# Optimization experiments

Hardware: AMD Instinct MI355X
Metric: run time of the kernel (lower is better)

## Reference

```python
import jax, jax.numpy as jnp
import numpy as np

BITS = 8
TOPK_PERCENT = 0.1
THRESHOLD = 0.5


def _quantize_per_channel(v, n_bits):
    # scales: abs-max over last dim, clamped, divided by q_max
    q_max = 2 ** (n_bits - 1) - 1
    scales = jnp.max(jnp.abs(v), axis=-1, keepdims=True)
    scales = jnp.clip(scales, 1e-5, None) / q_max
    return jnp.clip(jnp.round(v / scales), -q_max - 1, q_max) * scales


def setup_inputs() -> dict:
    key = jax.random.key(0)
    ks = jax.random.split(key, 5)
    B, S, D, H = 4, 2048, 1024, 4096
    return {
        "x": jax.random.normal(ks[0], (B, S, D), dtype=jnp.float32),
        "W1": jax.random.normal(ks[1], (H, D), dtype=jnp.float32) * 0.02,
        "b1": jax.random.normal(ks[2], (H,), dtype=jnp.float32) * 0.02,
        "W2": jax.random.normal(ks[3], (D, H), dtype=jnp.float32) * 0.02,
        "b2": jax.random.normal(ks[4], (D,), dtype=jnp.float32) * 0.02,
    }


def reference(x, W1, b1, W2, b2):
    D = W1.shape[-1]
    H = W1.shape[0]
    topk_rows = int(D * TOPK_PERCENT) + 1  # first-k-columns approximation

    # approximate preactivation using only the first topk_rows input channels
    prod_topk = jnp.einsum('bsk,hk->bsh', x[:, :, :topk_rows], W1[:, :topk_rows]) + b1
    # exact fp preactivation
    prod = jnp.einsum('bsd,hd->bsh', x, W1) + b1

    # quantized path: per-channel quant of x, W1, b1 then matmul
    q_x = _quantize_per_channel(x, BITS)
    q_w = _quantize_per_channel(W1, BITS)
    q_b = _quantize_per_channel(b1, BITS)
    q_pre = jnp.einsum('bsd,hd->bsh', q_x, q_w) + q_b

    # channel selection: channels predicted positive often enough stay fp
    threshold = prod_topk.shape[-1] * THRESHOLD
    num_pos_pred = jnp.sum(prod_topk > 0, axis=(0, 1))  # [H]
    fp_channels = num_pos_pred > threshold              # [H] bool

    h = jnp.where(fp_channels, prod, q_pre)
    h = jax.nn.gelu(h, approximate=False)
    out = jnp.einsum('bsh,dh->bsd', h, W2) + b2
    return out
```

## Files before the change

### kernel.cpp

```cpp
#include <hip/hip_runtime.h>
#include <math.h>
#include <stdint.h>


typedef __bf16 v8bf __attribute__((ext_vector_type(8)));
typedef float v4f __attribute__((ext_vector_type(4)));
typedef unsigned short v8us __attribute__((ext_vector_type(8)));

#define AS_G __attribute__((address_space(1)))
#define AS_L __attribute__((address_space(3)))
#define GLOAD(gp, lp) __builtin_amdgcn_global_load_lds((const AS_G void*)(gp), (AS_L void*)(lp), 16, 0, 0)
#define WAITV(n) asm volatile("s_waitcnt vmcnt(" #n ")" ::: "memory")
#define FENCE() __builtin_amdgcn_sched_barrier(0)
#define BAR() __builtin_amdgcn_s_barrier()

__device__ __forceinline__ unsigned short f2bf(float f) {
    union { float f; unsigned int i; } v; v.f = f;
    unsigned int r = v.i + 0x7fffu + ((v.i >> 16) & 1u);
    return (unsigned short)(r >> 16);
}
__device__ __forceinline__ float gelu_fast(float v) {
    float u = v * (0.79788456080286536f + 0.035677408136300125f * v * v);
    u = fminf(fmaxf(u, -15.f), 15.f);
    float e = __expf(2.0f * u);
    return v * e * __builtin_amdgcn_rcpf(e + 1.0f);
}
__device__ __forceinline__ float gelu_exact(float v) {
    return 0.5f * v * (1.0f + erff(v * 0.70710678118654752440f));
}

template<int NB>
__device__ __forceinline__ void gemm_core8(const unsigned short* __restrict__ A,
                                           const unsigned short* __restrict__ B,
                                           const int K, const int NC,
                                           const int bm0, const int bn0,
                                           unsigned short* lds,
                                           v4f (&acc)[8][NB / 4])
{
    constexpr int NF = NB / 4;
    constexpr int CH = (16 + NB) * 512;
    const int tid  = threadIdx.x;
    const int wave = tid >> 6;
    const int lane = tid & 63;
    const int wm = wave >> 2, wn = wave & 3;
    const int rowInChunk = lane >> 2;
    const int col8 = ((lane & 3) ^ ((lane >> 3) & 3)) * 8;
    const int ldsLane = lane * 8;
    const int R = lane & 15, Q = lane >> 4;
    const int roff = R * 32 + ((Q ^ ((R >> 1) & 3)) * 8);

    const size_t aR0 = (size_t)(bm0 + (2 * wave)     * 16 + rowInChunk) * K + col8;
    const size_t aR1 = (size_t)(bm0 + (2 * wave + 1) * 16 + rowInChunk) * K + col8;
    size_t bR0 = 0, bR1 = 0;
    if constexpr (NB == 16) {
        bR0 = (size_t)(bn0 + (2 * wave)     * 16 + rowInChunk) * K + col8;
        bR1 = (size_t)(bn0 + (2 * wave + 1) * 16 + rowInChunk) * K + col8;
    } else {
        bR0 = (size_t)(bn0 + wave * 16 + rowInChunk) * K + col8;
    }

    auto STAGE = [&](int kc, unsigned short* s) {
        const int k0 = kc * 32;
        GLOAD(A + aR0 + k0, s + (2 * wave) * 512 + ldsLane);
        GLOAD(A + aR1 + k0, s + (2 * wave + 1) * 512 + ldsLane);
        if constexpr (NB == 16) {
            GLOAD(B + bR0 + k0, s + (16 + 2 * wave) * 512 + ldsLane);
            GLOAD(B + bR1 + k0, s + (16 + 2 * wave + 1) * 512 + ldsLane);
        } else {
            GLOAD(B + bR0 + k0, s + (16 + wave) * 512 + ldsLane);
        }
    };
    auto COMPUTE = [&](const unsigned short* s) {
        v8bf af[8], bf[NF];
#pragma unroll
        for (int mf = 0; mf < 8; ++mf)
            af[mf] = *(const v8bf*)&s[(wm * 8 + mf) * 512 + roff];
#pragma unroll
        for (int nf = 0; nf < NF; ++nf)
            bf[nf] = *(const v8bf*)&s[(16 + wn * NF + nf) * 512 + roff];
        __builtin_amdgcn_s_setprio(1);
#pragma unroll
        for (int mf = 0; mf < 8; ++mf)
#pragma unroll
            for (int nf = 0; nf < NF; ++nf)
                acc[mf][nf] = __builtin_amdgcn_mfma_f32_16x16x32_bf16(af[mf], bf[nf], acc[mf][nf], 0, 0, 0);
        __builtin_amdgcn_s_setprio(0);
    };

    unsigned short* const sl3 = lds + 3 * (size_t)CH;
    STAGE(0, lds);
    STAGE(1, lds + CH);
    STAGE(2, lds + 2 * (size_t)CH);
    unsigned short* pc = lds;
    unsigned short* ps = sl3;

    for (int c = 0; c < NC - 3; ++c) {
        STAGE(c + 3, ps);
        if constexpr (NB == 16) WAITV(12); else WAITV(9);
        FENCE(); BAR(); FENCE();
        COMPUTE(pc);
        FENCE(); BAR(); FENCE();
        ps = pc;
        pc = (pc == sl3) ? lds : pc + CH;
    }
    if constexpr (NB == 16) WAITV(8); else WAITV(6);
    FENCE(); BAR(); FENCE();
    COMPUTE(pc);
    FENCE(); BAR(); FENCE();
    pc = (pc == sl3) ? lds : pc + CH;
    if constexpr (NB == 16) WAITV(4); else WAITV(3);
    FENCE(); BAR(); FENCE();
    COMPUTE(pc);
    FENCE(); BAR(); FENCE();
    pc = (pc == sl3) ? lds : pc + CH;
    WAITV(0);
    FENCE(); BAR(); FENCE();
    COMPUTE(pc);
    FENCE(); BAR(); FENCE();
}

__global__ void prep_kernel(const float* __restrict__ x, const float* __restrict__ W1,
                            const float* __restrict__ W2, const float* __restrict__ b1,
                            unsigned short* __restrict__ xb, unsigned short* __restrict__ w1b,
                            unsigned short* __restrict__ w2b,
                            unsigned short* __restrict__ xpad, unsigned short* __restrict__ w1pad,
                            float* __restrict__ s_x, float* __restrict__ s_w,
                            float* __restrict__ s_b, int* __restrict__ counts)
{
    const int b = blockIdx.x, t = threadIdx.x;
    __shared__ float red[4];

    if (b < 16384) {
        const float* src; unsigned short* dst; unsigned short* pad = nullptr; float* sc = nullptr;
        if (b < 8192)       { src = x  + (size_t)b * 1024;            dst = xb  + (size_t)b * 1024;
                              pad = xpad  + (size_t)b * 128;          sc = s_x + b; }
        else if (b < 12288) { int r = b - 8192;  src = W1 + (size_t)r * 1024; dst = w1b + (size_t)r * 1024;
                              pad = w1pad + (size_t)r * 128;          sc = s_w + r; }
        else                { int r = b - 12288; src = W2 + (size_t)r * 1024; dst = w2b + (size_t)r * 1024; }

        float4 v = ((const float4*)src)[t];
        ushort4 u;
        u.x = f2bf(v.x); u.y = f2bf(v.y); u.z = f2bf(v.z); u.w = f2bf(v.w);
        ((ushort4*)dst)[t] = u;
        if (pad && t < 32) {
            int c = t * 4;
            ushort4 p;
            p.x = (c + 0 < 103) ? u.x : (unsigned short)0;
            p.y = (c + 1 < 103) ? u.y : (unsigned short)0;
            p.z = (c + 2 < 103) ? u.z : (unsigned short)0;
            p.w = (c + 3 < 103) ? u.w : (unsigned short)0;
            ((ushort4*)pad)[t] = p;
        }
        if (sc) {
            float m = fmaxf(fmaxf(fabsf(v.x), fabsf(v.y)), fmaxf(fabsf(v.z), fabsf(v.w)));
#pragma unroll
            for (int off = 32; off; off >>= 1) m = fmaxf(m, __shfl_xor(m, off, 64));
            if ((t & 63) == 0) red[t >> 6] = m;
            __syncthreads();
            if (t == 0) {
                m = fmaxf(fmaxf(red[0], red[1]), fmaxf(red[2], red[3]));
                *sc = fmaxf(m, 1e-5f) * (1.0f / 127.0f);
            }
        }
    } else {
        float m = 0.f;
        for (int k = t; k < 4096; k += 256) { m = fmaxf(m, fabsf(b1[k])); counts[k] = 0; }
#pragma unroll
        for (int off = 32; off; off >>= 1) m = fmaxf(m, __shfl_xor(m, off, 64));
        if ((t & 63) == 0) red[t >> 6] = m;
        __syncthreads();
        if (t == 0) {
            m = fmaxf(fmaxf(red[0], red[1]), fmaxf(red[2], red[3]));
            *s_b = fmaxf(m, 1e-5f) * (1.0f / 127.0f);
        }
    }
}

__global__ __launch_bounds__(512, 2)
void gemm1_topk(const unsigned short* __restrict__ xb,
                const unsigned short* __restrict__ w1b,
                const unsigned short* __restrict__ xpad,
                const unsigned short* __restrict__ w1pad,
                const float* __restrict__ b1,
                unsigned short* __restrict__ hbuf,
                int* __restrict__ counts)
{
    __shared__ unsigned short lds[65536];
    v4f acc[8][4];
    v4f z = {0.f, 0.f, 0.f, 0.f};
#pragma unroll
    for (int i = 0; i < 8; ++i)
#pragma unroll
        for (int j = 0; j < 4; ++j) acc[i][j] = z;

    const int bn0 = blockIdx.x * 256, bm0 = blockIdx.y * 256;
    const int tid = threadIdx.x;
    const int lane = tid & 63, wave = tid >> 6;
    const int wm = wave >> 2, wn = wave & 3, q = lane >> 4;

    if (blockIdx.z == 0) {
        gemm_core8<16>(xb, w1b, 1024, 32, bm0, bn0, lds, acc);

        float bvj[4];
#pragma unroll
        for (int nf = 0; nf < 4; ++nf) bvj[nf] = b1[bn0 + wn * 64 + nf * 16 + (lane & 15)];

        unsigned short* slab = lds;
#pragma unroll
        for (int p = 0; p < 4; ++p) {
            __syncthreads();
            if (wm == (p >> 1)) {
                const int mfb = (p & 1) * 4;
#pragma unroll
                for (int mfp = 0; mfp < 4; ++mfp)
#pragma unroll
                    for (int nf = 0; nf < 4; ++nf) {
                        const int colq = wn * 64 + nf * 16 + (lane & 15);
#pragma unroll
                        for (int r = 0; r < 4; ++r)
                            slab[(mfp * 16 + q * 4 + r) * 256 + colq] =
                                f2bf(gelu_fast(acc[mfb + mfp][nf][r] + bvj[nf]));
                    }
            }
            __syncthreads();
#pragma unroll
            for (int s = 0; s < 4; ++s) {
                const int idx = s * 512 + tid;
                const int row = idx >> 5, ch = idx & 31;
                *(v8us*)&hbuf[(size_t)(bm0 + p * 64 + row) * 4096 + bn0 + ch * 8] =
                    *(const v8us*)&slab[row * 256 + ch * 8];
            }
        }
    } else {
        gemm_core8<16>(xpad, w1pad, 128, 4, bm0, bn0, lds, acc);

#pragma unroll
        for (int nf = 0; nf < 4; ++nf) {
            const int n = bn0 + wn * 64 + nf * 16 + (lane & 15);
            const float bv = b1[n];
            int cnt = 0;
#pragma unroll
            for (int mf = 0; mf < 8; ++mf)
#pragma unroll
                for (int r = 0; r < 4; ++r)
                    cnt += (acc[mf][nf][r] + bv > 0.0f) ? 1 : 0;
            cnt += __shfl_xor(cnt, 16, 64);
            cnt += __shfl_xor(cnt, 32, 64);
            if (lane < 16 && cnt) atomicAdd(&counts[n], cnt);
        }
    }
}

__global__ void fixup_kernel(const float* __restrict__ x,
                             const float* __restrict__ W1,
                             const float* __restrict__ b1,
                             const int* __restrict__ counts,
                             const float* __restrict__ s_x,
                             const float* __restrict__ s_w,
                             const float* __restrict__ s_b,
                             unsigned short* __restrict__ hbuf)
{
    const int n = blockIdx.x;
    if (counts[n] > 2048) return;
    __shared__ float qw[1024];
    const float swn = s_w[n];
    for (int k = threadIdx.x; k < 1024; k += 256) {
        float q = nearbyintf(W1[(size_t)n * 1024 + k] / swn);
        qw[k] = fminf(fmaxf(q, -128.f), 127.f) * swn;
    }
    __syncthreads();
    const float sb = *s_b;
    const float bq = fminf(fmaxf(nearbyintf(b1[n] / sb), -128.f), 127.f) * sb;
    for (int m = threadIdx.x; m < 8192; m += 256) {
        const float sxm = s_x[m];
        float a = 0.f;
        for (int k = 0; k < 1024; ++k) {
            float q = nearbyintf(x[(size_t)m * 1024 + k] / sxm);
            a += fminf(fmaxf(q, -128.f), 127.f) * sxm * qw[k];
        }
        hbuf[(size_t)m * 4096 + n] = f2bf(gelu_exact(a + bq));
    }
}

__global__ __launch_bounds__(512, 2)
void gemm2_bias(const unsigned short* __restrict__ hbuf,
                const unsigned short* __restrict__ w2b,
                const float* __restrict__ b2,
                float* __restrict__ out)
{
    __shared__ unsigned short lds[49152];
    v4f acc[8][2];
    v4f z = {0.f, 0.f, 0.f, 0.f};
#pragma unroll
    for (int i = 0; i < 8; ++i)
#pragma unroll
        for (int j = 0; j < 2; ++j) acc[i][j] = z;

    const int bn0 = blockIdx.x * 128, bm0 = blockIdx.y * 256;
    const int tid = threadIdx.x;
    const int lane = tid & 63, wave = tid >> 6;
    const int wm = wave >> 2, wn = wave & 3, q = lane >> 4;

    gemm_core8<8>(hbuf, w2b, 4096, 128, bm0, bn0, lds, acc);

    float bvj[2];
#pragma unroll
    for (int nf = 0; nf < 2; ++nf) bvj[nf] = b2[bn0 + wn * 32 + nf * 16 + (lane & 15)];

    float* slabf = (float*)lds;
#pragma unroll
    for (int p = 0; p < 4; ++p) {
        __syncthreads();
        if (wm == (p >> 1)) {
            const int mfb = (p & 1) * 4;
#pragma unroll
            for (int mfp = 0; mfp < 4; ++mfp)
#pragma unroll
                for (int nf = 0; nf < 2; ++nf) {
                    const int colq = wn * 32 + nf * 16 + (lane & 15);
#pragma unroll
                    for (int r = 0; r < 4; ++r)
                        slabf[(mfp * 16 + q * 4 + r) * 128 + colq] =
                            acc[mfb + mfp][nf][r] + bvj[nf];
                }
        }
        __syncthreads();
#pragma unroll
        for (int s = 0; s < 4; ++s) {
            const int idx = s * 512 + tid;
            const int row = idx >> 5, ch = idx & 31;
            *(float4*)&out[(size_t)(bm0 + p * 64 + row) * 1024 + bn0 + ch * 4] =
                *(const float4*)&slabf[row * 128 + ch * 4];
        }
    }
}

extern "C" void kernel_launch(void* const* d_in, const int* in_sizes, int n_in,
                              void* d_out, int out_size, void* d_ws, size_t ws_size,
                              hipStream_t stream)
{
    const float* x  = (const float*)d_in[0];
    const float* W1 = (const float*)d_in[1];
    const float* b1 = (const float*)d_in[2];
    const float* W2 = (const float*)d_in[3];
    const float* b2 = (const float*)d_in[4];
    float* out = (float*)d_out;

    unsigned short* xb  = (unsigned short*)d_out;
    unsigned short* w1b = (unsigned short*)d_out + (size_t)8192 * 1024;

    char* ws = (char*)d_ws;
    int*   counts = (int*)(ws + 0);
    float* s_x    = (float*)(ws + (64 << 10));
    float* s_w    = (float*)(ws + (96 << 10));
    float* s_b    = (float*)(ws + (112 << 10));
    unsigned short* xpad  = (unsigned short*)(ws + (1 << 20));
    unsigned short* w1pad = (unsigned short*)(ws + (3 << 20));
    unsigned short* w2b   = (unsigned short*)(ws + (4 << 20));
    unsigned short* hbuf  = (unsigned short*)(ws + (12 << 20));

    prep_kernel<<<16385, 256, 0, stream>>>(x, W1, W2, b1, xb, w1b, w2b,
                                           xpad, w1pad, s_x, s_w, s_b, counts);
    gemm1_topk<<<dim3(16, 32, 2), 512, 0, stream>>>(xb, w1b, xpad, w1pad, b1, hbuf, counts);
    fixup_kernel<<<4096, 256, 0, stream>>>(x, W1, b1, counts, s_x, s_w, s_b, hbuf);
    gemm2_bias<<<dim3(8, 32), 512, 0, stream>>>(hbuf, w2b, b2, out);
}
```

Baseline: 300.0 us.

## Restructure GEMM mainloop into double-buffered 64-wide K tiles with interleaved half-steps

Replaces the 4-stage ring of 32-wide K chunks with two 64-wide K tile buffers. Each tile is split into sub-steps where LDS fragment reads, async global-to-LDS loads for future tiles, and MFMA groups over half the N fragments are interleaved between barriers. The aim is finer overlap of memory traffic with matrix math and less LDS-read stalling. In exchange it adds many more barriers per K step and fragile hand-tuned vmcnt waits whose correctness depends on the exact load order.

```diff
diff --git a/kernel.cpp b/kernel.cpp
--- a/kernel.cpp
+++ b/kernel.cpp
@@ -30,93 +30,118 @@
 }
 
 template<int NB>
-__device__ __forceinline__ void gemm_core8(const unsigned short* __restrict__ A,
-                                           const unsigned short* __restrict__ B,
-                                           const int K, const int NC,
-                                           const int bm0, const int bn0,
-                                           unsigned short* lds,
-                                           v4f (&acc)[8][NB / 4])
+__device__ __forceinline__ void gemm_core8p(const unsigned short* __restrict__ A,
+                                            const unsigned short* __restrict__ Bm,
+                                            const int K,
+                                            const int bm0, const int bn0,
+                                            unsigned short* lds,
+                                            v4f (&acc)[8][NB / 4])
 {
     constexpr int NF = NB / 4;
-    constexpr int CH = (16 + NB) * 512;
-    const int tid  = threadIdx.x;
-    const int wave = tid >> 6;
-    const int lane = tid & 63;
+    constexpr int FW = NF / 2;
+    constexpr int TILE = (32 + 2 * NB) * 512;
+    const int tid = threadIdx.x;
+    const int wave = tid >> 6, lane = tid & 63;
     const int wm = wave >> 2, wn = wave & 3;
     const int rowInChunk = lane >> 2;
     const int col8 = ((lane & 3) ^ ((lane >> 3) & 3)) * 8;
     const int ldsLane = lane * 8;
     const int R = lane & 15, Q = lane >> 4;
     const int roff = R * 32 + ((Q ^ ((R >> 1) & 3)) * 8);
-
-    const size_t aR0 = (size_t)(bm0 + (2 * wave)     * 16 + rowInChunk) * K + col8;
-    const size_t aR1 = (size_t)(bm0 + (2 * wave + 1) * 16 + rowInChunk) * K + col8;
-    size_t bR0 = 0, bR1 = 0;
+    const int NT2 = K >> 7;
+
+    unsigned short* const buf0 = lds;
+    unsigned short* const buf1 = lds + TILE;
+
+    const size_t aB0 = (size_t)(bm0 + (2 * wave) * 16 + rowInChunk) * K + col8;
+    const size_t aB1 = aB0 + (size_t)16 * K;
+    size_t bB0, bB1 = 0;
     if constexpr (NB == 16) {
-        bR0 = (size_t)(bn0 + (2 * wave)     * 16 + rowInChunk) * K + col8;
-        bR1 = (size_t)(bn0 + (2 * wave + 1) * 16 + rowInChunk) * K + col8;
+        bB0 = (size_t)(bn0 + (2 * wave) * 16 + rowInChunk) * K + col8;
+        bB1 = bB0 + (size_t)16 * K;
     } else {
-        bR0 = (size_t)(bn0 + wave * 16 + rowInChunk) * K + col8;
-    }
-
-    auto STAGE = [&](int kc, unsigned short* s) {
-        const int k0 = kc * 32;
-        GLOAD(A + aR0 + k0, s + (2 * wave) * 512 + ldsLane);
-        GLOAD(A + aR1 + k0, s + (2 * wave + 1) * 512 + ldsLane);
-        if constexpr (NB == 16) {
-            GLOAD(B + bR0 + k0, s + (16 + 2 * wave) * 512 + ldsLane);
-            GLOAD(B + bR1 + k0, s + (16 + 2 * wave + 1) * 512 + ldsLane);
-        } else {
-            GLOAD(B + bR0 + k0, s + (16 + wave) * 512 + ldsLane);
-        }
-    };
-    auto COMPUTE = [&](const unsigned short* s) {
-        v8bf af[8], bf[NF];
-#pragma unroll
-        for (int mf = 0; mf < 8; ++mf)
-            af[mf] = *(const v8bf*)&s[(wm * 8 + mf) * 512 + roff];
-#pragma unroll
-        for (int nf = 0; nf < NF; ++nf)
-            bf[nf] = *(const v8bf*)&s[(16 + wn * NF + nf) * 512 + roff];
-        __builtin_amdgcn_s_setprio(1);
-#pragma unroll
-        for (int mf = 0; mf < 8; ++mf)
-#pragma unroll
-            for (int nf = 0; nf < NF; ++nf)
-                acc[mf][nf] = __builtin_amdgcn_mfma_f32_16x16x32_bf16(af[mf], bf[nf], acc[mf][nf], 0, 0, 0);
-        __builtin_amdgcn_s_setprio(0);
-    };
-
-    unsigned short* const sl3 = lds + 3 * (size_t)CH;
-    STAGE(0, lds);
-    STAGE(1, lds + CH);
-    STAGE(2, lds + 2 * (size_t)CH);
-    unsigned short* pc = lds;
-    unsigned short* ps = sl3;
-
-    for (int c = 0; c < NC - 3; ++c) {
-        STAGE(c + 3, ps);
-        if constexpr (NB == 16) WAITV(12); else WAITV(9);
-        FENCE(); BAR(); FENCE();
-        COMPUTE(pc);
-        FENCE(); BAR(); FENCE();
-        ps = pc;
-        pc = (pc == sl3) ? lds : pc + CH;
-    }
-    if constexpr (NB == 16) WAITV(8); else WAITV(6);
+        bB0 = (size_t)(bn0 + wave * 16 + rowInChunk) * K + col8;
+    }
+
+    v8bf Ar[8];
+    v8bf Br[FW];
+
+#define STG_A(tl, ks, bufp) { \
+    GLOAD(A + aB0 + (tl) * 64 + (ks) * 32, (bufp) + ((2 * wave) * 2 + (ks)) * 512 + ldsLane); \
+    GLOAD(A + aB1 + (tl) * 64 + (ks) * 32, (bufp) + ((2 * wave + 1) * 2 + (ks)) * 512 + ldsLane); }
+#define STG_B(tl, ks, bufp) { \
+    if constexpr (NB == 16) { \
+        GLOAD(Bm + bB0 + (tl) * 64 + (ks) * 32, (bufp) + 16384 + ((2 * wave) * 2 + (ks)) * 512 + ldsLane); \
+        GLOAD(Bm + bB1 + (tl) * 64 + (ks) * 32, (bufp) + 16384 + ((2 * wave + 1) * 2 + (ks)) * 512 + ldsLane); \
+    } else { \
+        GLOAD(Bm + bB0 + (tl) * 64 + (ks) * 32, (bufp) + 16384 + ((wave) * 2 + (ks)) * 512 + ldsLane); } }
+#define RD_A(bufp, ks) { _Pragma("unroll") \
+    for (int mf = 0; mf < 8; ++mf) \
+        Ar[mf] = *(const v8bf*)&(bufp)[((wm * 8 + mf) * 2 + (ks)) * 512 + roff]; }
+#define RD_B(bufp, ks, fg) { _Pragma("unroll") \
+    for (int nfi = 0; nfi < FW; ++nfi) \
+        Br[nfi] = *(const v8bf*)&(bufp)[16384 + ((wn * NF + (fg) * FW + nfi) * 2 + (ks)) * 512 + roff]; }
+#define MM(fg) \
+    __builtin_amdgcn_s_setprio(1); \
+    _Pragma("unroll") for (int mf = 0; mf < 8; ++mf) { \
+    _Pragma("unroll") for (int nfi = 0; nfi < FW; ++nfi) \
+        acc[mf][(fg) * FW + nfi] = __builtin_amdgcn_mfma_f32_16x16x32_bf16(Ar[mf], Br[nfi], acc[mf][(fg) * FW + nfi], 0, 0, 0); } \
+    __builtin_amdgcn_s_setprio(0);
+#define MIDB FENCE(); BAR(); FENCE();
+#define ENDB FENCE(); BAR(); FENCE();
+#define WVS  { if constexpr (NB == 16) { WAITV(10); } else { WAITV(8); } }
+
+    STG_A(0, 0, buf0); STG_B(0, 0, buf0); STG_A(0, 1, buf0); STG_B(0, 1, buf0);
+    STG_A(1, 0, buf1); STG_B(1, 0, buf1); STG_A(1, 1, buf1);
+    WVS;
     FENCE(); BAR(); FENCE();
-    COMPUTE(pc);
-    FENCE(); BAR(); FENCE();
-    pc = (pc == sl3) ? lds : pc + CH;
-    if constexpr (NB == 16) WAITV(4); else WAITV(3);
-    FENCE(); BAR(); FENCE();
-    COMPUTE(pc);
-    FENCE(); BAR(); FENCE();
-    pc = (pc == sl3) ? lds : pc + CH;
-    WAITV(0);
-    FENCE(); BAR(); FENCE();
-    COMPUTE(pc);
-    FENCE(); BAR(); FENCE();
+
+    for (int i = 0; i < NT2 - 1; ++i) {
+        const int t1 = 2 * i + 1, t2 = 2 * i + 2, t3 = 2 * i + 3;
+        RD_A(buf0, 0); RD_B(buf0, 0, 0); STG_B(t1, 1, buf1);
+        MIDB; MM(0); ENDB;
+        RD_B(buf0, 0, 1); STG_A(t2, 0, buf0);
+        MIDB; MM(1); WVS; ENDB;
+        RD_A(buf0, 1); RD_B(buf0, 1, 0); STG_B(t2, 0, buf0);
+        MIDB; MM(0); ENDB;
+        RD_B(buf0, 1, 1); STG_A(t2, 1, buf0);
+        MIDB; MM(1); WVS; ENDB;
+        RD_A(buf1, 0); RD_B(buf1, 0, 0); STG_B(t2, 1, buf0);
+        MIDB; MM(0); ENDB;
+        RD_B(buf1, 0, 1); STG_A(t3, 0, buf1);
+        MIDB; MM(1); WVS; ENDB;
+        RD_A(buf1, 1); RD_B(buf1, 1, 0); STG_B(t3, 0, buf1);
+        MIDB; MM(0); ENDB;
+        RD_B(buf1, 1, 1); STG_A(t3, 1, buf1);
+        MIDB; MM(1); WVS; ENDB;
+    }
+    {
+        const int tl = NT2 * 2 - 1;
+        RD_A(buf0, 0); RD_B(buf0, 0, 0); STG_B(tl, 1, buf1);
+        MIDB; MM(0); ENDB;
+        RD_B(buf0, 0, 1);
+        MIDB; MM(1); if constexpr (NB == 16) { WAITV(8); } else { WAITV(6); } ENDB;
+        RD_A(buf0, 1); RD_B(buf0, 1, 0);
+        MIDB; MM(0); ENDB;
+        RD_B(buf0, 1, 1);
+        MIDB; MM(1); if constexpr (NB == 16) { WAITV(4); } else { WAITV(3); } ENDB;
+        RD_A(buf1, 0); RD_B(buf1, 0, 0);
+        MIDB; MM(0); ENDB;
+        RD_B(buf1, 0, 1);
+        MIDB; MM(1); WAITV(0); ENDB;
+        RD_A(buf1, 1); RD_B(buf1, 1, 0);
+        MIDB; MM(0); ENDB;
+        RD_B(buf1, 1, 1);
+        MIDB; MM(1); ENDB;
+    }
+#undef STG_A
+#undef STG_B
+#undef RD_A
+#undef RD_B
+#undef MM
+#undef MIDB
+#undef ENDB
+#undef WVS
 }
 
 __global__ void prep_kernel(const float* __restrict__ x, const float* __restrict__ W1,
@@ -199,7 +224,7 @@
     const int wm = wave >> 2, wn = wave & 3, q = lane >> 4;
 
     if (blockIdx.z == 0) {
-        gemm_core8<16>(xb, w1b, 1024, 32, bm0, bn0, lds, acc);
+        gemm_core8p<16>(xb, w1b, 1024, bm0, bn0, lds, acc);
 
         float bvj[4];
 #pragma unroll
@@ -232,7 +257,7 @@
             }
         }
     } else {
-        gemm_core8<16>(xpad, w1pad, 128, 4, bm0, bn0, lds, acc);
+        gemm_core8p<16>(xpad, w1pad, 128, bm0, bn0, lds, acc);
 
 #pragma unroll
         for (int nf = 0; nf < 4; ++nf) {
@@ -301,7 +326,7 @@
     const int lane = tid & 63, wave = tid >> 6;
     const int wm = wave >> 2, wn = wave & 3, q = lane >> 4;
 
-    gemm_core8<8>(hbuf, w2b, 4096, 128, bm0, bn0, lds, acc);
+    gemm_core8p<8>(hbuf, w2b, 4096, bm0, bn0, lds, acc);
 
     float bvj[2];
 #pragma unroll
```

After: 300.3 us. About the same (+0.1%).

## Rework GEMM cores to 4-wave blocks with larger per-wave tiles and triple buffering

Applied to the files above, without the earlier changes.

Replaces the shared 8-wave GEMM core with two specialized 4-wave cores (256 threads). Each wave now computes a larger register tile (8x8 or 8x4 MFMA fragments), and B fragments are read in two halves interleaved with MFMA phases. The pipeline moves from a 4-deep to a 3-deep LDS ring, and gemm2 uses a K-step of 64 per stage. The goal is more operand reuse per LDS read and fewer waves sharing the barrier. In exchange, register pressure rises, each block has fewer waves to hide latency, and there are more barriers per K step.

```diff
diff --git a/kernel.cpp b/kernel.cpp
--- a/kernel.cpp
+++ b/kernel.cpp
@@ -29,94 +29,191 @@
     return 0.5f * v * (1.0f + erff(v * 0.70710678118654752440f));
 }
 
-template<int NB>
-__device__ __forceinline__ void gemm_core8(const unsigned short* __restrict__ A,
-                                           const unsigned short* __restrict__ B,
-                                           const int K, const int NC,
-                                           const int bm0, const int bn0,
-                                           unsigned short* lds,
-                                           v4f (&acc)[8][NB / 4])
-{
-    constexpr int NF = NB / 4;
-    constexpr int CH = (16 + NB) * 512;
-    const int tid  = threadIdx.x;
-    const int wave = tid >> 6;
-    const int lane = tid & 63;
-    const int wm = wave >> 2, wn = wave & 3;
+__device__ __forceinline__ void core_g1(const unsigned short* __restrict__ A,
+                                        const unsigned short* __restrict__ B,
+                                        const int K, const int bm0, const int bn0,
+                                        unsigned short* lds, v4f (&acc)[8][8])
+{
+    const int tid = threadIdx.x;
+    const int wave = tid >> 6, lane = tid & 63;
+    const int wm = wave & 1, wn = wave >> 1;
     const int rowInChunk = lane >> 2;
     const int col8 = ((lane & 3) ^ ((lane >> 3) & 3)) * 8;
     const int ldsLane = lane * 8;
     const int R = lane & 15, Q = lane >> 4;
     const int roff = R * 32 + ((Q ^ ((R >> 1) & 3)) * 8);
-
-    const size_t aR0 = (size_t)(bm0 + (2 * wave)     * 16 + rowInChunk) * K + col8;
-    const size_t aR1 = (size_t)(bm0 + (2 * wave + 1) * 16 + rowInChunk) * K + col8;
-    size_t bR0 = 0, bR1 = 0;
-    if constexpr (NB == 16) {
-        bR0 = (size_t)(bn0 + (2 * wave)     * 16 + rowInChunk) * K + col8;
-        bR1 = (size_t)(bn0 + (2 * wave + 1) * 16 + rowInChunk) * K + col8;
-    } else {
-        bR0 = (size_t)(bn0 + wave * 16 + rowInChunk) * K + col8;
-    }
-
-    auto STAGE = [&](int kc, unsigned short* s) {
-        const int k0 = kc * 32;
-        GLOAD(A + aR0 + k0, s + (2 * wave) * 512 + ldsLane);
-        GLOAD(A + aR1 + k0, s + (2 * wave + 1) * 512 + ldsLane);
-        if constexpr (NB == 16) {
-            GLOAD(B + bR0 + k0, s + (16 + 2 * wave) * 512 + ldsLane);
-            GLOAD(B + bR1 + k0, s + (16 + 2 * wave + 1) * 512 + ldsLane);
-        } else {
-            GLOAD(B + bR0 + k0, s + (16 + wave) * 512 + ldsLane);
-        }
-    };
-    auto COMPUTE = [&](const unsigned short* s) {
-        v8bf af[8], bf[NF];
-#pragma unroll
-        for (int mf = 0; mf < 8; ++mf)
-            af[mf] = *(const v8bf*)&s[(wm * 8 + mf) * 512 + roff];
-#pragma unroll
-        for (int nf = 0; nf < NF; ++nf)
-            bf[nf] = *(const v8bf*)&s[(16 + wn * NF + nf) * 512 + roff];
-        __builtin_amdgcn_s_setprio(1);
-#pragma unroll
-        for (int mf = 0; mf < 8; ++mf)
-#pragma unroll
-            for (int nf = 0; nf < NF; ++nf)
-                acc[mf][nf] = __builtin_amdgcn_mfma_f32_16x16x32_bf16(af[mf], bf[nf], acc[mf][nf], 0, 0, 0);
-        __builtin_amdgcn_s_setprio(0);
-    };
-
-    unsigned short* const sl3 = lds + 3 * (size_t)CH;
-    STAGE(0, lds);
-    STAGE(1, lds + CH);
-    STAGE(2, lds + 2 * (size_t)CH);
+    const int NS = K >> 5;
+
+    size_t aR[4], bR[4];
+#pragma unroll
+    for (int r = 0; r < 4; ++r) {
+        aR[r] = (size_t)(bm0 + (wave * 4 + r) * 16 + rowInChunk) * K + col8;
+        bR[r] = (size_t)(bn0 + (wave * 4 + r) * 16 + rowInChunk) * K + col8;
+    }
+
+    v8bf Ar[8], Br[4];
+
+#define G1_STG(c, s) { _Pragma("unroll") \
+    for (int r = 0; r < 4; ++r) { \
+        GLOAD(A + aR[r] + (c) * 32, (s) + (wave * 4 + r) * 512 + ldsLane); \
+        GLOAD(B + bR[r] + (c) * 32, (s) + 8192 + (wave * 4 + r) * 512 + ldsLane); } }
+#define G1_RDA(s) { _Pragma("unroll") \
+    for (int mf = 0; mf < 8; ++mf) \
+        Ar[mf] = *(const v8bf*)&(s)[(wm * 8 + mf) * 512 + roff]; }
+#define G1_RDB(s, fg) { _Pragma("unroll") \
+    for (int nf = 0; nf < 4; ++nf) \
+        Br[nf] = *(const v8bf*)&(s)[8192 + (wn * 8 + (fg) * 4 + nf) * 512 + roff]; }
+#define G1_MM(fg) \
+    __builtin_amdgcn_s_setprio(1); \
+    _Pragma("unroll") for (int mf = 0; mf < 8; ++mf) { \
+    _Pragma("unroll") for (int nf = 0; nf < 4; ++nf) \
+        acc[mf][(fg) * 4 + nf] = __builtin_amdgcn_mfma_f32_16x16x32_bf16(Ar[mf], Br[nf], acc[mf][(fg) * 4 + nf], 0, 0, 0); } \
+    __builtin_amdgcn_s_setprio(0);
+
     unsigned short* pc = lds;
-    unsigned short* ps = sl3;
-
-    for (int c = 0; c < NC - 3; ++c) {
-        STAGE(c + 3, ps);
-        if constexpr (NB == 16) WAITV(12); else WAITV(9);
-        FENCE(); BAR(); FENCE();
-        COMPUTE(pc);
-        FENCE(); BAR(); FENCE();
-        ps = pc;
-        pc = (pc == sl3) ? lds : pc + CH;
-    }
-    if constexpr (NB == 16) WAITV(8); else WAITV(6);
-    FENCE(); BAR(); FENCE();
-    COMPUTE(pc);
-    FENCE(); BAR(); FENCE();
-    pc = (pc == sl3) ? lds : pc + CH;
-    if constexpr (NB == 16) WAITV(4); else WAITV(3);
-    FENCE(); BAR(); FENCE();
-    COMPUTE(pc);
-    FENCE(); BAR(); FENCE();
-    pc = (pc == sl3) ? lds : pc + CH;
-    WAITV(0);
-    FENCE(); BAR(); FENCE();
-    COMPUTE(pc);
-    FENCE(); BAR(); FENCE();
+    unsigned short* pn = lds + 16384;
+    unsigned short* ps = lds + 32768;
+
+    G1_STG(0, pc); G1_STG(1, pn);
+    WAITV(8);
+    FENCE(); BAR(); FENCE();
+
+    for (int c = 0; c < NS - 2; ++c) {
+        G1_RDA(pc); G1_RDB(pc, 0); G1_STG(c + 2, ps);
+        FENCE(); BAR(); FENCE();
+        G1_MM(0);
+        FENCE(); BAR(); FENCE();
+        G1_RDB(pc, 1);
+        FENCE(); BAR(); FENCE();
+        G1_MM(1); WAITV(8);
+        FENCE(); BAR(); FENCE();
+        unsigned short* t = pc; pc = pn; pn = ps; ps = t;
+    }
+    G1_RDA(pc); G1_RDB(pc, 0);
+    FENCE(); BAR(); FENCE();
+    G1_MM(0);
+    FENCE(); BAR(); FENCE();
+    G1_RDB(pc, 1);
+    FENCE(); BAR(); FENCE();
+    G1_MM(1); WAITV(0);
+    FENCE(); BAR(); FENCE();
+    { unsigned short* t = pc; pc = pn; pn = ps; ps = t; }
+    G1_RDA(pc); G1_RDB(pc, 0);
+    FENCE(); BAR(); FENCE();
+    G1_MM(0);
+    FENCE(); BAR(); FENCE();
+    G1_RDB(pc, 1);
+    FENCE(); BAR(); FENCE();
+    G1_MM(1);
+    FENCE(); BAR(); FENCE();
+#undef G1_STG
+#undef G1_RDA
+#undef G1_RDB
+#undef G1_MM
+}
+
+__device__ __forceinline__ void core_g2(const unsigned short* __restrict__ A,
+                                        const unsigned short* __restrict__ B,
+                                        const int K, const int bm0, const int bn0,
+                                        unsigned short* lds, v4f (&acc)[8][4])
+{
+    const int tid = threadIdx.x;
+    const int wave = tid >> 6, lane = tid & 63;
+    const int wm = wave & 1, wn = wave >> 1;
+    const int rowInChunk = lane >> 2;
+    const int col8 = ((lane & 3) ^ ((lane >> 3) & 3)) * 8;
+    const int ldsLane = lane * 8;
+    const int R = lane & 15, Q = lane >> 4;
+    const int roff = R * 32 + ((Q ^ ((R >> 1) & 3)) * 8);
+    const int NS = K >> 6;
+
+    size_t aR[4], bR[2];
+#pragma unroll
+    for (int r = 0; r < 4; ++r)
+        aR[r] = (size_t)(bm0 + (wave * 4 + r) * 16 + rowInChunk) * K + col8;
+#pragma unroll
+    for (int r = 0; r < 2; ++r)
+        bR[r] = (size_t)(bn0 + (wave * 2 + r) * 16 + rowInChunk) * K + col8;
+
+    v8bf Ar[8], Br[2];
+
+#define G2_STG(c, s) { _Pragma("unroll") \
+    for (int r = 0; r < 4; ++r) { _Pragma("unroll") \
+        for (int ks = 0; ks < 2; ++ks) \
+            GLOAD(A + aR[r] + (c) * 64 + ks * 32, (s) + ((wave * 4 + r) * 2 + ks) * 512 + ldsLane); } \
+    _Pragma("unroll") \
+    for (int r = 0; r < 2; ++r) { _Pragma("unroll") \
+        for (int ks = 0; ks < 2; ++ks) \
+            GLOAD(B + bR[r] + (c) * 64 + ks * 32, (s) + 16384 + ((wave * 2 + r) * 2 + ks) * 512 + ldsLane); } }
+#define G2_RDA(s, ks) { _Pragma("unroll") \
+    for (int mf = 0; mf < 8; ++mf) \
+        Ar[mf] = *(const v8bf*)&(s)[((wm * 8 + mf) * 2 + (ks)) * 512 + roff]; }
+#define G2_RDB(s, ks, fg) { _Pragma("unroll") \
+    for (int nf = 0; nf < 2; ++nf) \
+        Br[nf] = *(const v8bf*)&(s)[16384 + ((wn * 4 + (fg) * 2 + nf) * 2 + (ks)) * 512 + roff]; }
+#define G2_MM(fg) \
+    __builtin_amdgcn_s_setprio(1); \
+    _Pragma("unroll") for (int mf = 0; mf < 8; ++mf) { \
+    _Pragma("unroll") for (int nf = 0; nf < 2; ++nf) \
+        acc[mf][(fg) * 2 + nf] = __builtin_amdgcn_mfma_f32_16x16x32_bf16(Ar[mf], Br[nf], acc[mf][(fg) * 2 + nf], 0, 0, 0); } \
+    __builtin_amdgcn_s_setprio(0);
+#define G2_PH(s, ks, fg) \
+    FENCE(); BAR(); FENCE(); \
+    G2_MM(fg); \
+    FENCE(); BAR(); FENCE();
+
+    unsigned short* pc = lds;
+    unsigned short* pn = lds + 24576;
+    unsigned short* ps = lds + 49152;
+
+    G2_STG(0, pc); G2_STG(1, pn);
+    WAITV(12);
+    FENCE(); BAR(); FENCE();
+
+    for (int c = 0; c < NS - 2; ++c) {
+        G2_RDA(pc, 0); G2_RDB(pc, 0, 0); G2_STG(c + 2, ps);
+        FENCE(); BAR(); FENCE();
+        G2_MM(0);
+        FENCE(); BAR(); FENCE();
+        G2_RDB(pc, 0, 1);
+        FENCE(); BAR(); FENCE();
+        G2_MM(1);
+        FENCE(); BAR(); FENCE();
+        G2_RDA(pc, 1); G2_RDB(pc, 1, 0);
+        FENCE(); BAR(); FENCE();
+        G2_MM(0);
+        FENCE(); BAR(); FENCE();
+        G2_RDB(pc, 1, 1);
+        FENCE(); BAR(); FENCE();
+        G2_MM(1); WAITV(12);
+        FENCE(); BAR(); FENCE();
+        unsigned short* t = pc; pc = pn; pn = ps; ps = t;
+    }
+    for (int c = 0; c < 2; ++c) {
+        G2_RDA(pc, 0); G2_RDB(pc, 0, 0);
+        FENCE(); BAR(); FENCE();
+        G2_MM(0);
+        FENCE(); BAR(); FENCE();
+        G2_RDB(pc, 0, 1);
+        FENCE(); BAR(); FENCE();
+        G2_MM(1);
+        FENCE(); BAR(); FENCE();
+        G2_RDA(pc, 1); G2_RDB(pc, 1, 0);
+        FENCE(); BAR(); FENCE();
+        G2_MM(0);
+        FENCE(); BAR(); FENCE();
+        G2_RDB(pc, 1, 1);
+        FENCE(); BAR(); FENCE();
+        G2_MM(1);
+        if (c == 0) { WAITV(0); }
+        FENCE(); BAR(); FENCE();
+        unsigned short* t = pc; pc = pn; pn = ps; ps = t;
+    }
+#undef G2_STG
+#undef G2_RDA
+#undef G2_RDB
+#undef G2_MM
+#undef G2_PH
 }
 
 __global__ void prep_kernel(const float* __restrict__ x, const float* __restrict__ W1,
@@ -176,7 +273,7 @@
     }
 }
 
-__global__ __launch_bounds__(512, 2)
+__global__ __launch_bounds__(256, 1)
 void gemm1_topk(const unsigned short* __restrict__ xb,
                 const unsigned short* __restrict__ w1b,
                 const unsigned short* __restrict__ xpad,
@@ -185,25 +282,26 @@
                 unsigned short* __restrict__ hbuf,
                 int* __restrict__ counts)
 {
-    __shared__ unsigned short lds[65536];
-    v4f acc[8][4];
+    __shared__ unsigned short lds[49152];
+    v4f acc[8][8];
     v4f z = {0.f, 0.f, 0.f, 0.f};
 #pragma unroll
     for (int i = 0; i < 8; ++i)
 #pragma unroll
-        for (int j = 0; j < 4; ++j) acc[i][j] = z;
+        for (int j = 0; j < 8; ++j) acc[i][j] = z;
 
     const int bn0 = blockIdx.x * 256, bm0 = blockIdx.y * 256;
     const int tid = threadIdx.x;
     const int lane = tid & 63, wave = tid >> 6;
-    const int wm = wave >> 2, wn = wave & 3, q = lane >> 4;
+    const int wm = wave & 1, wn = wave >> 1, q = lane >> 4;
+    const int R = lane & 15;
 
     if (blockIdx.z == 0) {
-        gemm_core8<16>(xb, w1b, 1024, 32, bm0, bn0, lds, acc);
-
-        float bvj[4];
-#pragma unroll
-        for (int nf = 0; nf < 4; ++nf) bvj[nf] = b1[bn0 + wn * 64 + nf * 16 + (lane & 15)];
+        core_g1(xb, w1b, 1024, bm0, bn0, lds, acc);
+
+        float bvj[8];
+#pragma unroll
+        for (int nf = 0; nf < 8; ++nf) bvj[nf] = b1[bn0 + wn * 128 + nf * 16 + R];
 
         unsigned short* slab = lds;
 #pragma unroll
@@ -214,8 +312,8 @@
 #pragma unroll
                 for (int mfp = 0; mfp < 4; ++mfp)
 #pragma unroll
-                    for (int nf = 0; nf < 4; ++nf) {
-                        const int colq = wn * 64 + nf * 16 + (lane & 15);
+                    for (int nf = 0; nf < 8; ++nf) {
+                        const int colq = wn * 128 + nf * 16 + R;
 #pragma unroll
                         for (int r = 0; r < 4; ++r)
                             slab[(mfp * 16 + q * 4 + r) * 256 + colq] =
@@ -224,19 +322,19 @@
             }
             __syncthreads();
 #pragma unroll
-            for (int s = 0; s < 4; ++s) {
-                const int idx = s * 512 + tid;
+            for (int s = 0; s < 8; ++s) {
+                const int idx = s * 256 + tid;
                 const int row = idx >> 5, ch = idx & 31;
                 *(v8us*)&hbuf[(size_t)(bm0 + p * 64 + row) * 4096 + bn0 + ch * 8] =
                     *(const v8us*)&slab[row * 256 + ch * 8];
             }
         }
     } else {
-        gemm_core8<16>(xpad, w1pad, 128, 4, bm0, bn0, lds, acc);
-
-#pragma unroll
-        for (int nf = 0; nf < 4; ++nf) {
-            const int n = bn0 + wn * 64 + nf * 16 + (lane & 15);
+        core_g1(xpad, w1pad, 128, bm0, bn0, lds, acc);
+
+#pragma unroll
+        for (int nf = 0; nf < 8; ++nf) {
+            const int n = bn0 + wn * 128 + nf * 16 + R;
             const float bv = b1[n];
             int cnt = 0;
 #pragma unroll
@@ -282,30 +380,31 @@
     }
 }
 
-__global__ __launch_bounds__(512, 2)
+__global__ __launch_bounds__(256, 1)
 void gemm2_bias(const unsigned short* __restrict__ hbuf,
                 const unsigned short* __restrict__ w2b,
                 const float* __restrict__ b2,
                 float* __restrict__ out)
 {
-    __shared__ unsigned short lds[49152];
-    v4f acc[8][2];
+    __shared__ unsigned short lds[73728];
+    v4f acc[8][4];
     v4f z = {0.f, 0.f, 0.f, 0.f};
 #pragma unroll
     for (int i = 0; i < 8; ++i)
 #pragma unroll
-        for (int j = 0; j < 2; ++j) acc[i][j] = z;
+        for (int j = 0; j < 4; ++j) acc[i][j] = z;
 
     const int bn0 = blockIdx.x * 128, bm0 = blockIdx.y * 256;
     const int tid = threadIdx.x;
     const int lane = tid & 63, wave = tid >> 6;
-    const int wm = wave >> 2, wn = wave & 3, q = lane >> 4;
-
-    gemm_core8<8>(hbuf, w2b, 4096, 128, bm0, bn0, lds, acc);
-
-    float bvj[2];
-#pragma unroll
-    for (int nf = 0; nf < 2; ++nf) bvj[nf] = b2[bn0 + wn * 32 + nf * 16 + (lane & 15)];
+    const int wm = wave & 1, wn = wave >> 1, q = lane >> 4;
+    const int R = lane & 15;
+
+    core_g2(hbuf, w2b, 4096, bm0, bn0, lds, acc);
+
+    float bvj[4];
+#pragma unroll
+    for (int nf = 0; nf < 4; ++nf) bvj[nf] = b2[bn0 + wn * 64 + nf * 16 + R];
 
     float* slabf = (float*)lds;
 #pragma unroll
@@ -316,8 +415,8 @@
 #pragma unroll
             for (int mfp = 0; mfp < 4; ++mfp)
 #pragma unroll
-                for (int nf = 0; nf < 2; ++nf) {
-                    const int colq = wn * 32 + nf * 16 + (lane & 15);
+                for (int nf = 0; nf < 4; ++nf) {
+                    const int colq = wn * 64 + nf * 16 + R;
 #pragma unroll
                     for (int r = 0; r < 4; ++r)
                         slabf[(mfp * 16 + q * 4 + r) * 128 + colq] =
@@ -326,8 +425,8 @@
         }
         __syncthreads();
 #pragma unroll
-        for (int s = 0; s < 4; ++s) {
-            const int idx = s * 512 + tid;
+        for (int s = 0; s < 8; ++s) {
+            const int idx = s * 256 + tid;
             const int row = idx >> 5, ch = idx & 31;
             *(float4*)&out[(size_t)(bm0 + p * 64 + row) * 1024 + bn0 + ch * 4] =
                 *(const float4*)&slabf[row * 128 + ch * 4];
@@ -361,7 +460,7 @@
 
     prep_kernel<<<16385, 256, 0, stream>>>(x, W1, W2, b1, xb, w1b, w2b,
                                            xpad, w1pad, s_x, s_w, s_b, counts);
-    gemm1_topk<<<dim3(16, 32, 2), 512, 0, stream>>>(xb, w1b, xpad, w1pad, b1, hbuf, counts);
+    gemm1_topk<<<dim3(16, 32, 2), 256, 0, stream>>>(xb, w1b, xpad, w1pad, b1, hbuf, counts);
     fixup_kernel<<<4096, 256, 0, stream>>>(x, W1, b1, counts, s_x, s_w, s_b, hbuf);
-    gemm2_bias<<<dim3(8, 32), 512, 0, stream>>>(hbuf, w2b, b2, out);
-}
+    gemm2_bias<<<dim3(8, 32), 256, 0, stream>>>(hbuf, w2b, b2, out);
+}
```

After: 349.3 us. 1.16x slower.
